# Performance work log

Measured on AMD Instinct MI355X. Metric: run time of the kernel, lower is better.

## Reference

```python
import jax, jax.numpy as jnp
import numpy as np

N = 50000      # nodes
E = 800000     # edges
FIN = 128      # num_feature
EDIM = 16      # edge_dim
OUT = 64       # out_dim (per-head channels; concat=False averages heads)
H = 4          # heads
SCALE = 1.0 / float(np.sqrt(OUT))


def _layernorm(h, g, b):
    mu = h.mean(-1, keepdims=True)
    var = ((h - mu) ** 2).mean(-1, keepdims=True)
    return (h - mu) * jax.lax.rsqrt(var + 1e-5) * g + b


def _tconv(x, src, dst, ea, Wq, bq, Wk, bk, Wv, bv, We, Ws, bs):
    # PyG TransformerConv, concat=False, root_weight=True, eval mode (no dropout)
    n = x.shape[0]
    q = (x @ Wq + bq).reshape(n, H, OUT)[dst]   # [E,H,D] query at destination
    k = (x @ Wk + bk).reshape(n, H, OUT)[src]   # [E,H,D] key at source
    v = (x @ Wv + bv).reshape(n, H, OUT)[src]   # [E,H,D] value at source
    e = (ea @ We).reshape(-1, H, OUT)           # [E,H,D] edge embedding (no bias)
    logits = jnp.einsum('ehd,ehd->eh', q, k + e) * SCALE   # [E,H]
    # segment softmax over incoming edges of each destination node
    m = jax.lax.stop_gradient(jax.ops.segment_max(logits, dst, num_segments=n))
    a = jnp.exp(logits - m[dst])
    s = jax.ops.segment_sum(a, dst, num_segments=n)
    alpha = a / s[dst]                                     # [E,H]
    agg = jax.ops.segment_sum((v + e) * alpha[..., None], dst, num_segments=n)  # [N,H,D]
    return agg.mean(axis=1) + x @ Ws + bs      # concat=False -> head mean; + skip


def _forward(x, src, dst, ea, p1, p2, p3, g, b):
    h = x
    for p in (p1, p2, p3):
        h = jax.nn.gelu(_layernorm(_tconv(h, src, dst, ea, *p), g, b), approximate=False)
    return h


def setup_inputs() -> dict:
    key = jax.random.key(0)
    ks = iter(jax.random.split(key, 64))
    def nrm(shp, s=0.05):
        return jax.random.normal(next(ks), shp, jnp.float32) * s
    inp = {
        'x': nrm((N, FIN), 1.0),
        'edge_index': jax.random.randint(next(ks), (2, E), 0, N),
        'edge_attr': nrm((E, EDIM), 1.0),
    }
    for l, fin in ((1, FIN), (2, OUT), (3, OUT)):
        inp[f'Wq{l}'] = nrm((fin, H * OUT)); inp[f'bq{l}'] = jnp.zeros((H * OUT,), jnp.float32)
        inp[f'Wk{l}'] = nrm((fin, H * OUT)); inp[f'bk{l}'] = jnp.zeros((H * OUT,), jnp.float32)
        inp[f'Wv{l}'] = nrm((fin, H * OUT)); inp[f'bv{l}'] = jnp.zeros((H * OUT,), jnp.float32)
        inp[f'We{l}'] = nrm((EDIM, H * OUT))
        inp[f'Ws{l}'] = nrm((fin, OUT)); inp[f'bs{l}'] = jnp.zeros((OUT,), jnp.float32)
    inp['ln_g'] = jnp.ones((OUT,), jnp.float32)
    inp['ln_b'] = jnp.zeros((OUT,), jnp.float32)
    return inp


def reference(x, edge_index, edge_attr,
              Wq1, bq1, Wk1, bk1, Wv1, bv1, We1, Ws1, bs1,
              Wq2, bq2, Wk2, bk2, Wv2, bv2, We2, Ws2, bs2,
              Wq3, bq3, Wk3, bk3, Wv3, bv3, We3, Ws3, bs3,
              ln_g, ln_b):
    src, dst = edge_index[0], edge_index[1]
    p1 = (Wq1, bq1, Wk1, bk1, Wv1, bv1, We1, Ws1, bs1)
    p2 = (Wq2, bq2, Wk2, bk2, Wv2, bv2, We2, Ws2, bs2)
    p3 = (Wq3, bq3, Wk3, bk3, Wv3, bv3, We3, Ws3, bs3)
    return _forward(x, src, dst, edge_attr, p1, p2, p3, ln_g, ln_b)
```

## Files before the change

kernel.cpp:

```cpp
#include <hip/hip_runtime.h>
#include <hip/hip_bf16.h>
#include <math.h>

#define NNODES 50000
#define NEDGES 800000
#define HD     256
#define CW     384
#define NTOT   896
#define QS     0.18033688011112042f

typedef __hip_bfloat16 bf16;
typedef unsigned short u16;
typedef unsigned char  u8;
typedef unsigned int   u32;
typedef __attribute__((ext_vector_type(8))) short bf16x8;
typedef __attribute__((ext_vector_type(4))) float f32x4;
typedef __attribute__((ext_vector_type(2))) float f32x2;

__device__ __forceinline__ float lo16f(u32 u) { return __uint_as_float(u << 16); }
__device__ __forceinline__ float hi16f(u32 u) { return __uint_as_float(u & 0xFFFF0000u); }
__device__ __forceinline__ short f2s(float v) { __hip_bfloat16 h = __float2bfloat16(v); return *(short*)&h; }

__device__ __forceinline__ void gload_lds16(const void* g, void* l) {
    __builtin_amdgcn_global_load_lds(
        (const __attribute__((address_space(1))) void*)g,
        (__attribute__((address_space(3))) void*)l, 16, 0, 0);
}

template<int CTRL>
__device__ __forceinline__ float dppadd(float x) {
    int t = __builtin_amdgcn_update_dpp(0, __float_as_int(x), CTRL, 0xF, 0xF, true);
    return x + __int_as_float(t);
}

__global__ void hist_kernel(const int* __restrict__ dst, int* __restrict__ deg, int E) {
    int e = blockIdx.x * 256 + threadIdx.x;
    if (e < E) atomicAdd(&deg[dst[e]], 1);
}

__global__ void scanA(const int* __restrict__ deg, int* __restrict__ locincl,
                      int* __restrict__ blocksum, int n) {
    int tid = threadIdx.x;
    int i = blockIdx.x * 256 + tid;
    int v = (i < n) ? deg[i] : 0;
    int lane = tid & 63, w = tid >> 6;
    int s = v;
    #pragma unroll
    for (int off = 1; off < 64; off <<= 1) {
        int t = __shfl_up(s, off);
        if (lane >= off) s += t;
    }
    __shared__ int wsum[4];
    if (lane == 63) wsum[w] = s;
    __syncthreads();
    for (int ww = 0; ww < w; ww++) s += wsum[ww];
    if (i < n) locincl[i] = s;
    if (tid == 255) blocksum[blockIdx.x] = s;
}

__global__ void scanB(const int* __restrict__ blocksum, int* __restrict__ blockoff,
                      int nb, int* __restrict__ rowptr, int n) {
    int tid = threadIdx.x;
    int v = (tid < nb) ? blocksum[tid] : 0;
    int lane = tid & 63, w = tid >> 6;
    int s = v;
    #pragma unroll
    for (int off = 1; off < 64; off <<= 1) {
        int t = __shfl_up(s, off);
        if (lane >= off) s += t;
    }
    __shared__ int wsum[4];
    if (lane == 63) wsum[w] = s;
    __syncthreads();
    for (int ww = 0; ww < w; ww++) s += wsum[ww];
    if (tid < nb) blockoff[tid] = s - v;
    if (tid == 255) rowptr[n] = s;
}

__global__ void scanC(const int* __restrict__ deg, const int* __restrict__ locincl,
                      const int* __restrict__ blockoff,
                      int* __restrict__ rowptr, int* __restrict__ cursor, int n) {
    int i = blockIdx.x * 256 + threadIdx.x;
    if (i < n) {
        int ex = locincl[i] - deg[i] + blockoff[blockIdx.x];
        rowptr[i] = ex;
        cursor[i] = ex;
    }
}

__global__ void scatter_kernel(const int* __restrict__ src, const int* __restrict__ dst,
                               int* __restrict__ cursor, int2* __restrict__ csr2, int E) {
    int e = blockIdx.x * 256 + threadIdx.x;
    if (e < E) {
        int d = dst[e];
        int p = atomicAdd(&cursor[d], 1);
        csr2[p] = make_int2(src[e], e);
    }
}

__global__ void xcast(const float* __restrict__ x, u16* __restrict__ xb) {
    int i = blockIdx.x * 256 + threadIdx.x;
    const float4* p = (const float4*)(x + (size_t)i * 8);
    float4 a = p[0], b = p[1];
    union { u16 s[8]; uint4 u; } t;
    t.s[0] = (u16)f2s(a.x); t.s[1] = (u16)f2s(a.y); t.s[2] = (u16)f2s(a.z); t.s[3] = (u16)f2s(a.w);
    t.s[4] = (u16)f2s(b.x); t.s[5] = (u16)f2s(b.y); t.s[6] = (u16)f2s(b.z); t.s[7] = (u16)f2s(b.w);
    *(uint4*)(xb + (size_t)i * 8) = t.u;
}

__global__ void pack_all(const float* __restrict__ Wq, const float* __restrict__ bq,
                         const float* __restrict__ Wk, const float* __restrict__ bk,
                         const float* __restrict__ Wv, const float* __restrict__ bv,
                         const float* __restrict__ We,
                         const float* __restrict__ Ws, const float* __restrict__ bs,
                         bf16* __restrict__ Wc, float* __restrict__ b, int K) {
    int n = blockIdx.x, c = threadIdx.x;
    float v, bb;
    if (n < 256)      { v = Wq[(size_t)c * 256 + n] * QS;    bb = bq[n] * QS; }
    else if (n < 320) {
        int t = n - 256, h = t >> 4, j = t & 15;
        float s = 0.f, sb = 0.f;
        #pragma unroll 8
        for (int d = 0; d < 64; d++) {
            float wv = We[j * HD + h * 64 + d];
            s += Wq[(size_t)c * 256 + h * 64 + d] * wv;
            sb += bq[h * 64 + d] * wv;
        }
        v = s * QS; bb = sb * QS;
    }
    else if (n < 384) { v = Ws[(size_t)c * 64  + (n - 320)]; bb = bs[n - 320]; }
    else if (n < 640) { v = Wv[(size_t)c * 256 + (n - 384)]; bb = bv[n - 384]; }
    else              { v = Wk[(size_t)c * 256 + (n - 640)]; bb = bk[n - 640]; }
    Wc[(size_t)n * K + c] = __float2bfloat16(v);
    if (c == 0) b[n] = bb;
}

template<int K>
__global__ void __launch_bounds__(256) gemm_v4(
    const u16* __restrict__ A, const bf16* __restrict__ Wc, const float* __restrict__ bias,
    bf16* __restrict__ comb, bf16* __restrict__ vbuf, u8* __restrict__ k8)
{
    constexpr int KS    = K / 32;
    constexpr int ITERS = 4;
    constexpr int ROWB  = K * 2;
    constexpr int TILEB = 64 * ROWB;
    constexpr int WSEG  = TILEB / 4;
    constexpr int NINST = WSEG / 1024;
    __shared__ __align__(16) u8 Ab[2][TILEB];
    __shared__ __align__(16) u8 TrB[4][2560];
    int tid = threadIdx.x, w = tid >> 6, lane = tid & 63;
    int cl = lane & 15, aq = lane >> 4;
    int chunk = blockIdx.x;
    int slab = blockIdx.y * (64 * ITERS);
    u8* myT = TrB[w];

    bf16x8 bfr[4][KS];
    #pragma unroll
    for (int t = 0; t < 4; t++)
        #pragma unroll
        for (int ks = 0; ks < KS; ks++)
            bfr[t][ks] = *(const bf16x8*)((const u16*)Wc +
                         (size_t)(chunk * 64 + t * 16 + cl) * K + ks * 32 + aq * 8);

    float4 bv[4];
    #pragma unroll
    for (int t = 0; t < 4; t++) bv[t] = *(const float4*)&bias[chunk * 64 + t * 16 + aq * 4];

    auto STAGE = [&](int b, int it) {
        int m0 = slab + it * 64;
        #pragma unroll
        for (int i = 0; i < NINST; i++) {
            int off = w * WSEG + i * 1024;
            int rowbase = off / ROWB;
            int row, gran;
            if constexpr (K == 64) { row = rowbase + (lane >> 3); gran = lane & 7;  }
            else                   { row = rowbase + (lane >> 4); gran = lane & 15; }
            int gr = m0 + row; if (gr >= NNODES) gr = NNODES - 1;
            int sg = gran ^ (row & 7);
            gload_lds16((const u8*)A + (size_t)gr * ROWB + sg * 16, Ab[b] + off);
        }
    };

    STAGE(0, 0);
    __syncthreads();
    int cur = 0;
    #pragma unroll
    for (int it = 0; it < ITERS; it++) {
        if (it + 1 < ITERS) STAGE(cur ^ 1, it + 1);

        int rowt = w * 16 + cl;
        bf16x8 a[KS];
        #pragma unroll
        for (int ks = 0; ks < KS; ks++)
            a[ks] = *(const bf16x8*)&Ab[cur][rowt * ROWB + (((ks * 4 + aq) ^ (rowt & 7)) << 4)];

        f32x4 acc[4] = {};
        #pragma unroll
        for (int t = 0; t < 4; t++)
            #pragma unroll
            for (int ks = 0; ks < KS; ks++)
                acc[t] = __builtin_amdgcn_mfma_f32_16x16x32_bf16(bfr[t][ks], a[ks], acc[t], 0, 0, 0);

        if (chunk < 10) {
            #pragma unroll
            for (int t = 0; t < 4; t++) {
                u32 lo = (u32)(u16)f2s(acc[t][0] + bv[t].x) | ((u32)(u16)f2s(acc[t][1] + bv[t].y) << 16);
                u32 hi = (u32)(u16)f2s(acc[t][2] + bv[t].z) | ((u32)(u16)f2s(acc[t][3] + bv[t].w) << 16);
                *(uint2*)(myT + cl * 160 + t * 32 + aq * 8) = make_uint2(lo, hi);
            }
            #pragma unroll
            for (int i = 0; i < 2; i++) {
                int r = i * 8 + (lane >> 3);
                uint4 vv = *(const uint4*)(myT + r * 160 + (lane & 7) * 16);
                int gr = slab + it * 64 + w * 16 + r;
                if (gr < NNODES) {
                    u16* dst = (chunk < 6) ? (u16*)comb + (size_t)gr * CW + chunk * 64
                                           : (u16*)vbuf + (size_t)gr * 256 + (chunk - 6) * 64;
                    *(uint4*)(dst + (lane & 7) * 8) = vv;
                }
            }
        } else {
            #pragma unroll
            for (int t = 0; t < 4; t++) {
                u32 pk = __builtin_amdgcn_cvt_pk_fp8_f32(acc[t][0] + bv[t].x, acc[t][1] + bv[t].y, 0, false);
                pk = __builtin_amdgcn_cvt_pk_fp8_f32(acc[t][2] + bv[t].z, acc[t][3] + bv[t].w, pk, true);
                *(u32*)(myT + cl * 80 + (t * 4 + aq) * 4) = pk;
            }
            {
                int r = lane >> 2;
                uint4 vv = *(const uint4*)(myT + r * 80 + (lane & 3) * 16);
                int gr = slab + it * 64 + w * 16 + r;
                if (gr < NNODES)
                    *(uint4*)(k8 + (size_t)gr * 256 + (chunk - 10) * 64 + (lane & 3) * 16) = vv;
            }
        }
        __syncthreads();
        cur ^= 1;
    }
}

__global__ void __launch_bounds__(256) node_fused(
    const int* __restrict__ rowptr, const int2* __restrict__ csr2,
    const float* __restrict__ eattr, const u16* __restrict__ comb,
    const u16* __restrict__ vbuf, const u8* __restrict__ k8,
    const float* __restrict__ We, const float* __restrict__ lng, const float* __restrict__ lnb,
    bf16* __restrict__ outB, float* __restrict__ outF)
{
    int tid = threadIdx.x, w = tid >> 6, lane = tid & 63;
    int n = blockIdx.x * 4 + w;
    int hg = lane >> 4, j16 = lane & 15, coff = 4 * lane;
    __shared__ float sAV[4][256];
    __shared__ float sAE[4][64];

    const u16* crow = comb + (size_t)n * CW;
    uint2 qv = *(const uint2*)(crow + coff);
    float qf0 = lo16f(qv.x), qf1 = hi16f(qv.x), qf2 = lo16f(qv.y), qf3 = hi16f(qv.y);
    float qwe_r = __uint_as_float((u32)crow[256 + lane] << 16);

    int e0 = __builtin_amdgcn_readfirstlane(rowptr[n]);
    int e1 = __builtin_amdgcn_readfirstlane(rowptr[n + 1]);

    float ss = 0.f, av0 = 0.f, av1 = 0.f, av2 = 0.f, av3 = 0.f, ae = 0.f;
    u32 vo = (u32)coff * 2u;
    u32 eo = (u32)j16 * 4u;

    auto EDGE = [&](int2 me) {
        u32 s   = (u32)__builtin_amdgcn_readfirstlane(me.x);
        u32 eid = (u32)__builtin_amdgcn_readfirstlane(me.y);
        const char* kp = (const char*)k8    + ((size_t)s << 8);
        const char* vp = (const char*)vbuf  + ((size_t)s << 9);
        const char* ep = (const char*)eattr + ((size_t)eid << 6);
        u32   kw = *(const u32*)  (kp + coff);
        uint2 vw = *(const uint2*)(vp + vo);
        float ea = *(const float*)(ep + eo);
        f32x2 k01 = __builtin_amdgcn_cvt_pk_f32_fp8(kw, false);
        f32x2 k23 = __builtin_amdgcn_cvt_pk_f32_fp8(kw, true);
        float part = qf0 * k01[0] + qf1 * k01[1] + qf2 * k23[0] + qf3 * k23[1] + qwe_r * ea;
        part = dppadd<0xB1>(part);
        part = dppadd<0x4E>(part);
        part = dppadd<0x141>(part);
        part = dppadd<0x140>(part);
        float alpha = __builtin_amdgcn_exp2f(part);
        ss += alpha;
        ae += alpha * ea;
        av0 += alpha * lo16f(vw.x); av1 += alpha * hi16f(vw.x);
        av2 += alpha * lo16f(vw.y); av3 += alpha * hi16f(vw.y);
    };

    int i = e0;
    int2 c0 = make_int2(0, 0), c1 = c0, c2 = c0, c3 = c0;
    if (i + 3 < e1) { c0 = csr2[i]; c1 = csr2[i + 1]; c2 = csr2[i + 2]; c3 = csr2[i + 3]; }
    for (; i + 7 < e1; i += 4) {
        int2 p0 = csr2[i + 4], p1 = csr2[i + 5], p2 = csr2[i + 6], p3 = csr2[i + 7];
        EDGE(c0); EDGE(c1); EDGE(c2); EDGE(c3);
        c0 = p0; c1 = p1; c2 = p2; c3 = p3;
    }
    if (i + 3 < e1) { EDGE(c0); EDGE(c1); EDGE(c2); EDGE(c3); i += 4; }
    for (; i < e1; ++i) { int2 cc = csr2[i]; EDGE(cc); }

    float inv = (ss > 0.f) ? 1.f / ss : 0.f;
    *(float4*)&sAV[w][coff] = make_float4(av0 * inv, av1 * inv, av2 * inv, av3 * inv);
    sAE[w][lane] = ae * inv;

    int d = lane;
    float val = 0.f;
    #pragma unroll
    for (int h = 0; h < 4; h++) {
        float xv = sAV[w][h * 64 + d];
        #pragma unroll
        for (int j = 0; j < 16; j++) xv += sAE[w][h * 16 + j] * We[j * HD + h * 64 + d];
        val += xv;
    }
    val = val * 0.25f + __uint_as_float((u32)crow[320 + d] << 16);

    float m = val;
    #pragma unroll
    for (int off = 1; off < 64; off <<= 1) m += __shfl_xor(m, off);
    m *= (1.f / 64.f);
    float diff = val - m;
    float vr = diff * diff;
    #pragma unroll
    for (int off = 1; off < 64; off <<= 1) vr += __shfl_xor(vr, off);
    vr *= (1.f / 64.f);
    float y = diff * rsqrtf(vr + 1e-5f) * lng[d] + lnb[d];
    float ge = 0.5f * y * (1.f + erff(y * 0.70710678118654752f));
    if (outF) outF[(size_t)n * 64 + d] = ge;
    else      outB[(size_t)n * 64 + d] = __float2bfloat16(ge);
}

extern "C" void kernel_launch(void* const* d_in, const int* in_sizes, int n_in,
                              void* d_out, int out_size, void* d_ws, size_t ws_size,
                              hipStream_t stream)
{
    const float* x     = (const float*)d_in[0];
    const int*   eidx  = (const int*)d_in[1];
    const float* eattr = (const float*)d_in[2];
    struct P { const float *Wq,*bq,*Wk,*bk,*Wv,*bv,*We,*Ws,*bs; };
    P p[3];
    for (int l = 0; l < 3; l++) {
        int base = 3 + l * 9;
        p[l].Wq = (const float*)d_in[base + 0]; p[l].bq = (const float*)d_in[base + 1];
        p[l].Wk = (const float*)d_in[base + 2]; p[l].bk = (const float*)d_in[base + 3];
        p[l].Wv = (const float*)d_in[base + 4]; p[l].bv = (const float*)d_in[base + 5];
        p[l].We = (const float*)d_in[base + 6];
        p[l].Ws = (const float*)d_in[base + 7]; p[l].bs = (const float*)d_in[base + 8];
    }
    const float* lng = (const float*)d_in[30];
    const float* lnb = (const float*)d_in[31];

    char* ws = (char*)d_ws;
    size_t off = 0;
    auto alloc = [&](size_t bytes) { void* pp = ws + off; off += (bytes + 255) & ~(size_t)255; return pp; };
    int*   rowptr   = (int*)  alloc((NNODES + 1) * 4);
    int*   cursor   = (int*)  alloc(NNODES * 4);
    int*   deg      = (int*)  alloc(NNODES * 4);
    int*   blocksum = (int*)  alloc(256 * 4);
    int*   blockoff = (int*)  alloc(256 * 4);
    int2*  csr2     = (int2*) alloc((size_t)NEDGES * 8);
    bf16*  hbuf     = (bf16*) alloc((size_t)NNODES * 64 * 2);
    u16*   xb       = (u16*)  alloc((size_t)NNODES * 128 * 2);
    bf16*  comb     = (bf16*) alloc((size_t)NNODES * CW * 2);
    bf16*  vbuf     = (bf16*) alloc((size_t)NNODES * 256 * 2);
    u8*    k8       = (u8*)   alloc((size_t)NNODES * 256);
    bf16*  Wc       = (bf16*) alloc((size_t)NTOT * 128 * 2);
    float* b896     = (float*)alloc(NTOT * 4);
    (void)ws_size;

    const int* srcArr = eidx;
    const int* dstArr = eidx + NEDGES;

    int NB = (NNODES + 255) / 256;
    (void)hipMemsetAsync(deg, 0, NNODES * 4, stream);
    hist_kernel<<<(NEDGES + 255) / 256, 256, 0, stream>>>(dstArr, deg, NEDGES);
    scanA<<<NB, 256, 0, stream>>>(deg, cursor, blocksum, NNODES);
    scanB<<<1, 256, 0, stream>>>(blocksum, blockoff, NB, rowptr, NNODES);
    scanC<<<NB, 256, 0, stream>>>(deg, cursor, blockoff, rowptr, cursor, NNODES);
    scatter_kernel<<<(NEDGES + 255) / 256, 256, 0, stream>>>(srcArr, dstArr, cursor, csr2, NEDGES);
    xcast<<<(NNODES * 128 / 8 + 255) / 256, 256, 0, stream>>>(x, xb);

    int NBY = (NNODES + 255) / 256;
    int fins[3] = {128, 64, 64};

    const u16* hin = xb;
    for (int l = 0; l < 3; l++) {
        int FIN = fins[l];
        pack_all<<<NTOT, FIN, 0, stream>>>(p[l].Wq, p[l].bq, p[l].Wk, p[l].bk,
                                           p[l].Wv, p[l].bv, p[l].We, p[l].Ws, p[l].bs,
                                           Wc, b896, FIN);
        if (l == 0) gemm_v4<128><<<dim3(14, NBY), 256, 0, stream>>>(hin, Wc, b896, comb, vbuf, k8);
        else        gemm_v4<64> <<<dim3(14, NBY), 256, 0, stream>>>(hin, Wc, b896, comb, vbuf, k8);
        node_fused<<<NNODES / 4, 256, 0, stream>>>(rowptr, csr2, eattr, (const u16*)comb,
            (const u16*)vbuf, k8, p[l].We, lng, lnb,
            (l == 2) ? nullptr : hbuf, (l == 2) ? (float*)d_out : nullptr);
        hin = (const u16*)hbuf;
    }
}
```

Before: 654.2 us.

## Permute edge attributes to CSR order in bf16 and interleave V/K rows

Measured after the change: 662.1 us. Within noise of the previous version (+1.2%).

```diff
diff --git a/kernel.cpp b/kernel.cpp
--- a/kernel.cpp
+++ b/kernel.cpp
@@ -89,13 +89,26 @@
 }
 
 __global__ void scatter_kernel(const int* __restrict__ src, const int* __restrict__ dst,
-                               int* __restrict__ cursor, int2* __restrict__ csr2, int E) {
+                               int* __restrict__ cursor,
+                               int* __restrict__ csr_src, int* __restrict__ csr_eid, int E) {
     int e = blockIdx.x * 256 + threadIdx.x;
     if (e < E) {
         int d = dst[e];
         int p = atomicAdd(&cursor[d], 1);
-        csr2[p] = make_int2(src[e], e);
-    }
+        csr_src[p] = src[e];
+        csr_eid[p] = e;
+    }
+}
+
+__global__ void eperm(const int* __restrict__ csr_eid, const float* __restrict__ eattr,
+                      u16* __restrict__ eattr_c) {
+    int g = blockIdx.x * 256 + threadIdx.x;
+    int p = g >> 2, part = g & 3;
+    int eid = csr_eid[p];
+    float4 v = *(const float4*)((const u8*)eattr + (size_t)eid * 64 + part * 16);
+    union { u16 s[4]; uint2 u; } t;
+    t.s[0] = (u16)f2s(v.x); t.s[1] = (u16)f2s(v.y); t.s[2] = (u16)f2s(v.z); t.s[3] = (u16)f2s(v.w);
+    *(uint2*)((u8*)eattr_c + (size_t)p * 32 + part * 8) = t.u;
 }
 
 __global__ void xcast(const float* __restrict__ x, u16* __restrict__ xb) {
@@ -138,7 +151,7 @@
 template<int K>
 __global__ void __launch_bounds__(256) gemm_v4(
     const u16* __restrict__ A, const bf16* __restrict__ Wc, const float* __restrict__ bias,
-    bf16* __restrict__ comb, bf16* __restrict__ vbuf, u8* __restrict__ k8)
+    bf16* __restrict__ comb, u8* __restrict__ kv)
 {
     constexpr int KS    = K / 32;
     constexpr int ITERS = 4;
@@ -214,9 +227,9 @@
                 uint4 vv = *(const uint4*)(myT + r * 160 + (lane & 7) * 16);
                 int gr = slab + it * 64 + w * 16 + r;
                 if (gr < NNODES) {
-                    u16* dst = (chunk < 6) ? (u16*)comb + (size_t)gr * CW + chunk * 64
-                                           : (u16*)vbuf + (size_t)gr * 256 + (chunk - 6) * 64;
-                    *(uint4*)(dst + (lane & 7) * 8) = vv;
+                    u8* dst = (chunk < 6) ? (u8*)comb + (size_t)gr * (CW * 2) + chunk * 128
+                                          : kv + (size_t)gr * 768 + (chunk - 6) * 128;
+                    *(uint4*)(dst + (lane & 7) * 16) = vv;
                 }
             }
         } else {
@@ -231,7 +244,7 @@
                 uint4 vv = *(const uint4*)(myT + r * 80 + (lane & 3) * 16);
                 int gr = slab + it * 64 + w * 16 + r;
                 if (gr < NNODES)
-                    *(uint4*)(k8 + (size_t)gr * 256 + (chunk - 10) * 64 + (lane & 3) * 16) = vv;
+                    *(uint4*)(kv + (size_t)gr * 768 + 512 + (chunk - 10) * 64 + (lane & 3) * 16) = vv;
             }
         }
         __syncthreads();
@@ -240,9 +253,9 @@
 }
 
 __global__ void __launch_bounds__(256) node_fused(
-    const int* __restrict__ rowptr, const int2* __restrict__ csr2,
-    const float* __restrict__ eattr, const u16* __restrict__ comb,
-    const u16* __restrict__ vbuf, const u8* __restrict__ k8,
+    const int* __restrict__ rowptr, const int* __restrict__ csr_src,
+    const u16* __restrict__ eattr_c, const u16* __restrict__ comb,
+    const u8* __restrict__ kv,
     const float* __restrict__ We, const float* __restrict__ lng, const float* __restrict__ lnb,
     bf16* __restrict__ outB, float* __restrict__ outF)
 {
@@ -262,17 +275,14 @@
 
     float ss = 0.f, av0 = 0.f, av1 = 0.f, av2 = 0.f, av3 = 0.f, ae = 0.f;
     u32 vo = (u32)coff * 2u;
-    u32 eo = (u32)j16 * 4u;
-
-    auto EDGE = [&](int2 me) {
-        u32 s   = (u32)__builtin_amdgcn_readfirstlane(me.x);
-        u32 eid = (u32)__builtin_amdgcn_readfirstlane(me.y);
-        const char* kp = (const char*)k8    + ((size_t)s << 8);
-        const char* vp = (const char*)vbuf  + ((size_t)s << 9);
-        const char* ep = (const char*)eattr + ((size_t)eid << 6);
-        u32   kw = *(const u32*)  (kp + coff);
-        uint2 vw = *(const uint2*)(vp + vo);
-        float ea = *(const float*)(ep + eo);
+    u32 eo = (u32)j16 * 2u;
+
+    auto EDGE = [&](int sm, int pos) {
+        u32 s = (u32)__builtin_amdgcn_readfirstlane(sm);
+        const u8* kvp = kv + (size_t)s * 768u;
+        uint2 vw = *(const uint2*)(kvp + vo);
+        u32   kw = *(const u32*)  (kvp + 512u + (u32)coff);
+        float ea = lo16f((u32)*(const u16*)((const u8*)eattr_c + (size_t)(u32)pos * 32u + eo));
         f32x2 k01 = __builtin_amdgcn_cvt_pk_f32_fp8(kw, false);
         f32x2 k23 = __builtin_amdgcn_cvt_pk_f32_fp8(kw, true);
         float part = qf0 * k01[0] + qf1 * k01[1] + qf2 * k23[0] + qf3 * k23[1] + qwe_r * ea;
@@ -287,16 +297,26 @@
         av2 += alpha * lo16f(vw.y); av3 += alpha * hi16f(vw.y);
     };
 
+    const int* cs = csr_src;
     int i = e0;
-    int2 c0 = make_int2(0, 0), c1 = c0, c2 = c0, c3 = c0;
-    if (i + 3 < e1) { c0 = csr2[i]; c1 = csr2[i + 1]; c2 = csr2[i + 2]; c3 = csr2[i + 3]; }
-    for (; i + 7 < e1; i += 4) {
-        int2 p0 = csr2[i + 4], p1 = csr2[i + 5], p2 = csr2[i + 6], p3 = csr2[i + 7];
-        EDGE(c0); EDGE(c1); EDGE(c2); EDGE(c3);
-        c0 = p0; c1 = p1; c2 = p2; c3 = p3;
-    }
-    if (i + 3 < e1) { EDGE(c0); EDGE(c1); EDGE(c2); EDGE(c3); i += 4; }
-    for (; i < e1; ++i) { int2 cc = csr2[i]; EDGE(cc); }
+    int m0 = 0, m1 = 0, m2 = 0, m3 = 0, m4 = 0, m5 = 0, m6 = 0, m7 = 0;
+    if (i + 7 < e1) {
+        m0 = cs[i];     m1 = cs[i + 1]; m2 = cs[i + 2]; m3 = cs[i + 3];
+        m4 = cs[i + 4]; m5 = cs[i + 5]; m6 = cs[i + 6]; m7 = cs[i + 7];
+    }
+    for (; i + 15 < e1; i += 8) {
+        int n0 = cs[i + 8],  n1 = cs[i + 9],  n2 = cs[i + 10], n3 = cs[i + 11];
+        int n4 = cs[i + 12], n5 = cs[i + 13], n6 = cs[i + 14], n7 = cs[i + 15];
+        EDGE(m0, i);     EDGE(m1, i + 1); EDGE(m2, i + 2); EDGE(m3, i + 3);
+        EDGE(m4, i + 4); EDGE(m5, i + 5); EDGE(m6, i + 6); EDGE(m7, i + 7);
+        m0 = n0; m1 = n1; m2 = n2; m3 = n3; m4 = n4; m5 = n5; m6 = n6; m7 = n7;
+    }
+    if (i + 7 < e1) {
+        EDGE(m0, i);     EDGE(m1, i + 1); EDGE(m2, i + 2); EDGE(m3, i + 3);
+        EDGE(m4, i + 4); EDGE(m5, i + 5); EDGE(m6, i + 6); EDGE(m7, i + 7);
+        i += 8;
+    }
+    for (; i < e1; ++i) EDGE(cs[i], i);
 
     float inv = (ss > 0.f) ? 1.f / ss : 0.f;
     *(float4*)&sAV[w][coff] = make_float4(av0 * inv, av1 * inv, av2 * inv, av3 * inv);
@@ -356,12 +376,13 @@
     int*   deg      = (int*)  alloc(NNODES * 4);
     int*   blocksum = (int*)  alloc(256 * 4);
     int*   blockoff = (int*)  alloc(256 * 4);
-    int2*  csr2     = (int2*) alloc((size_t)NEDGES * 8);
+    int*   csr_src  = (int*)  alloc((size_t)NEDGES * 4);
+    int*   csr_eid  = (int*)  alloc((size_t)NEDGES * 4);
+    u16*   eattr_c  = (u16*)  alloc((size_t)NEDGES * 16 * 2);
     bf16*  hbuf     = (bf16*) alloc((size_t)NNODES * 64 * 2);
     u16*   xb       = (u16*)  alloc((size_t)NNODES * 128 * 2);
     bf16*  comb     = (bf16*) alloc((size_t)NNODES * CW * 2);
-    bf16*  vbuf     = (bf16*) alloc((size_t)NNODES * 256 * 2);
-    u8*    k8       = (u8*)   alloc((size_t)NNODES * 256);
+    u8*    kv       = (u8*)   alloc((size_t)NNODES * 768);
     bf16*  Wc       = (bf16*) alloc((size_t)NTOT * 128 * 2);
     float* b896     = (float*)alloc(NTOT * 4);
     (void)ws_size;
@@ -375,7 +396,8 @@
     scanA<<<NB, 256, 0, stream>>>(deg, cursor, blocksum, NNODES);
     scanB<<<1, 256, 0, stream>>>(blocksum, blockoff, NB, rowptr, NNODES);
     scanC<<<NB, 256, 0, stream>>>(deg, cursor, blockoff, rowptr, cursor, NNODES);
-    scatter_kernel<<<(NEDGES + 255) / 256, 256, 0, stream>>>(srcArr, dstArr, cursor, csr2, NEDGES);
+    scatter_kernel<<<(NEDGES + 255) / 256, 256, 0, stream>>>(srcArr, dstArr, cursor, csr_src, csr_eid, NEDGES);
+    eperm<<<(4 * NEDGES) / 256, 256, 0, stream>>>(csr_eid, eattr, eattr_c);
     xcast<<<(NNODES * 128 / 8 + 255) / 256, 256, 0, stream>>>(x, xb);
 
     int NBY = (NNODES + 255) / 256;
@@ -387,10 +409,10 @@
         pack_all<<<NTOT, FIN, 0, stream>>>(p[l].Wq, p[l].bq, p[l].Wk, p[l].bk,
                                            p[l].Wv, p[l].bv, p[l].We, p[l].Ws, p[l].bs,
                                            Wc, b896, FIN);
-        if (l == 0) gemm_v4<128><<<dim3(14, NBY), 256, 0, stream>>>(hin, Wc, b896, comb, vbuf, k8);
-        else        gemm_v4<64> <<<dim3(14, NBY), 256, 0, stream>>>(hin, Wc, b896, comb, vbuf, k8);
-        node_fused<<<NNODES / 4, 256, 0, stream>>>(rowptr, csr2, eattr, (const u16*)comb,
-            (const u16*)vbuf, k8, p[l].We, lng, lnb,
+        if (l == 0) gemm_v4<128><<<dim3(14, NBY), 256, 0, stream>>>(hin, Wc, b896, comb, kv);
+        else        gemm_v4<64> <<<dim3(14, NBY), 256, 0, stream>>>(hin, Wc, b896, comb, kv);
+        node_fused<<<NNODES / 4, 256, 0, stream>>>(rowptr, csr_src, eattr_c, (const u16*)comb,
+            kv, p[l].We, lng, lnb,
             (l == 2) ? nullptr : hbuf, (l == 2) ? (float*)d_out : nullptr);
         hin = (const u16*)hbuf;
     }
```
